# Performance work log

Measured on AMD Instinct MI355X. Metric: run time of the kernel, lower is better.

Reference implementation:

```python
import jax, jax.numpy as jnp
import numpy as np


def setup_inputs() -> dict:
    key = jax.random.key(0)
    k1, k2, k3, k4, k5 = jax.random.split(key, 5)
    M, K, N, E = 16384, 2048, 5632, 8  # total_tokens, d_model, expert ffn dim, num_experts
    a = jax.random.normal(k1, (M, K), jnp.float32) * 0.1          # fp8-valued activations (simulated in f32)
    b = jax.random.normal(k2, (E, N, K), jnp.float32) * 0.05      # column-major expert weights [E, N, K]
    scale_a = jax.random.uniform(k3, (M, 1), jnp.float32, 0.5, 1.5)   # per-token dequant scale
    scale_b = jax.random.uniform(k4, (E, 1), jnp.float32, 0.5, 1.5)   # per-expert dequant scale
    cuts = jnp.sort(jax.random.randint(k5, (E - 1,), 0, M)).astype(jnp.int32)
    seg_indptr = jnp.concatenate([jnp.zeros(1, jnp.int32), cuts, jnp.full((1,), M, jnp.int32)])
    return {"a": a, "b": b, "scale_a": scale_a, "scale_b": scale_b,
            "seg_indptr": seg_indptr, "batch_size": E}


def reference(a, b, scale_a, scale_b, seg_indptr, batch_size):
    # Grouped GEMM: for expert e, rows seg_indptr[e]:seg_indptr[e+1] of `a` are
    # multiplied by b[e]^T (b is column-major [E, N, K]).
    M = a.shape[0]
    E = b.shape[0]
    group_sizes = jnp.diff(seg_indptr).astype(jnp.int32)           # [E]
    out = jax.lax.ragged_dot(a, jnp.swapaxes(b, 1, 2), group_sizes)  # [M, N]
    # fp8 w8a8 dequant: per-token scale_a, per-expert scale_b gathered per token
    eid = jnp.clip(jnp.searchsorted(seg_indptr, jnp.arange(M), side='right') - 1, 0, E - 1)
    return out * scale_a * scale_b[eid]
```

## Files before the change

### kernel.cpp

```cpp
#include <hip/hip_runtime.h>


#define KSLICE 32
#define NSLICE 64
#define BM 256
#define BN 256

typedef __attribute__((ext_vector_type(4))) float f32x4;
typedef __attribute__((ext_vector_type(4))) unsigned int u32x4;
using frag_ab = __attribute__((ext_vector_type(8))) short;
using frag_cd = __attribute__((ext_vector_type(4))) float;

__device__ __forceinline__ unsigned int pack_bf2(float x, float y) {
  unsigned int ux = __float_as_uint(x);
  unsigned int uy = __float_as_uint(y);
  ux += 0x7fffu + ((ux >> 16) & 1u);
  uy += 0x7fffu + ((uy >> 16) & 1u);
  return (ux >> 16) | (uy & 0xffff0000u);
}

__device__ __forceinline__ void gload_lds16(const void* g, void* lds) {
  __builtin_amdgcn_global_load_lds(
      (const __attribute__((address_space(1))) unsigned int*)g,
      (__attribute__((address_space(3))) unsigned int*)lds, 16, 0, 0);
}

__global__ __launch_bounds__(256)
void convert_kernel(const float* __restrict__ A, const float* __restrict__ B,
                    unsigned short* __restrict__ wa, unsigned short* __restrict__ wb) {
  constexpr long long NA = 16384LL * 2048;
  constexpr long long NB = 8LL * 5632 * 2048;
  constexpr long long NA8 = NA / 8;
  constexpr long long NTOT = (NA + NB) / 8;
  for (long long c = (long long)blockIdx.x * 256 + threadIdx.x; c < NTOT;
       c += (long long)gridDim.x * 256) {
    const float* src;
    unsigned short* dst;
    long long off;
    if (c < NA8) { src = A; dst = wa; off = c * 8; }
    else         { src = B; dst = wb; off = (c - NA8) * 8; }
    f32x4 v0 = *(const f32x4*)(src + off);
    f32x4 v1 = *(const f32x4*)(src + off + 4);
    u32x4 o;
    o[0] = pack_bf2(v0[0], v0[1]);
    o[1] = pack_bf2(v0[2], v0[3]);
    o[2] = pack_bf2(v1[0], v1[1]);
    o[3] = pack_bf2(v1[2], v1[3]);
    *(u32x4*)(dst + off) = o;
  }
}

__global__ __launch_bounds__(512, 2)
void ggemm8(const unsigned short* __restrict__ A,
            const unsigned short* __restrict__ B,
            const float* __restrict__ sa,
            const float* __restrict__ sb,
            const int* __restrict__ seg,
            float* __restrict__ C) {
  constexpr int M = 16384, K = 2048, N = 5632, E = 8;
  constexpr int NT = N / BN;
  const int nwg = (M / BM) * NT;

  int bid = blockIdx.x;
  int sid = (bid & 7) * (nwg >> 3) + (bid >> 3);
  int mt = sid / NT, nt = sid % NT;
  int m0 = mt * BM, n0 = nt * BN;

  int tid = threadIdx.x;
  int lane = tid & 63;
  int w = tid >> 6;
  int wrow = (w >> 2) * 128;
  int wcol = (w & 3) * 64;
  int l16 = lane & 15, lhi = lane >> 4;

  __shared__ unsigned short Alds[4 * 8192];
  __shared__ unsigned short Blds[4 * 8192];

  int rpl = lane >> 3;
  int slog = (lane & 7) ^ rpl;
  int srow = rpl * 2 + (slog >> 2);
  int sk0 = (slog & 3) * 8;
  const unsigned short* gA0 = A + (size_t)(m0 + w * 32 + srow) * K + sk0;
  const unsigned short* gA1 = gA0 + (size_t)16 * K;
  unsigned short* ldsA0 = &Alds[(w * 2 + 0) * 512];
  unsigned short* ldsA1 = &Alds[(w * 2 + 1) * 512];
  unsigned short* ldsB0 = &Blds[(w * 2 + 0) * 512];
  unsigned short* ldsB1 = &Blds[(w * 2 + 1) * 512];

  int offA[8], offB[4];
#pragma unroll
  for (int i = 0; i < 8; ++i) {
    int r = wrow + i * 16 + l16;
    int rp = r >> 1;
    int sl = ((r & 1) << 2) | lhi;
    offA[i] = rp * 64 + ((sl ^ (rp & 7)) << 3);
  }
#pragma unroll
  for (int j = 0; j < 4; ++j) {
    int r = wcol + j * 16 + l16;
    int rp = r >> 1;
    int sl = ((r & 1) << 2) | lhi;
    offB[j] = rp * 64 + ((sl ^ (rp & 7)) << 3);
  }

  for (int e = 0; e < E; ++e) {
    int rlo = max(m0, seg[e]);
    int rhi = min(m0 + BM, seg[e + 1]);
    if (rlo >= rhi) continue;

    const unsigned short* gB0 =
        B + (size_t)e * N * K + (size_t)(n0 + w * 32 + srow) * K + sk0;
    const unsigned short* gB1 = gB0 + (size_t)16 * K;

    frag_cd acc[8][4];
#pragma unroll
    for (int i = 0; i < 8; ++i)
#pragma unroll
      for (int j = 0; j < 4; ++j) acc[i][j] = (frag_cd){0.f, 0.f, 0.f, 0.f};

    auto stage = [&](int s) {
      int slot = (s & 3) * 8192;
      int g = s * KSLICE;
      gload_lds16(gA0 + g, ldsA0 + slot);
      gload_lds16(gA1 + g, ldsA1 + slot);
      gload_lds16(gB0 + g, ldsB0 + slot);
      gload_lds16(gB1 + g, ldsB1 + slot);
    };

    auto phase = [&](int s, auto vmwait) {
      int slot = (s & 3) * 8192;
      frag_ab af[8], bf[4];
#pragma unroll
      for (int i = 0; i < 8; ++i)
        af[i] = *(const frag_ab*)(&Alds[slot + offA[i]]);
#pragma unroll
      for (int j = 0; j < 4; ++j)
        bf[j] = *(const frag_ab*)(&Blds[slot + offB[j]]);
      if (s + 3 < NSLICE) stage(s + 3);
      vmwait();
      __builtin_amdgcn_s_barrier();
      asm volatile("s_waitcnt lgkmcnt(0)" ::: "memory");
      __builtin_amdgcn_s_setprio(1);
#pragma unroll
      for (int i = 0; i < 8; ++i)
#pragma unroll
        for (int j = 0; j < 4; ++j)
          acc[i][j] = __builtin_amdgcn_mfma_f32_16x16x32_bf16(
              af[i], bf[j], acc[i][j], 0, 0, 0);
      __builtin_amdgcn_s_setprio(0);
      __builtin_amdgcn_s_barrier();
    };

    auto W8 = [] { asm volatile("s_waitcnt vmcnt(8)" ::: "memory"); };
    auto W4 = [] { asm volatile("s_waitcnt vmcnt(4)" ::: "memory"); };
    auto W0 = [] { asm volatile("s_waitcnt vmcnt(0)" ::: "memory"); };

    stage(0); stage(1); stage(2);
    asm volatile("s_waitcnt vmcnt(8)" ::: "memory");
    __builtin_amdgcn_s_barrier();

#pragma unroll 4
    for (int s = 0; s < NSLICE - 4; ++s) phase(s, W8);
    phase(NSLICE - 4, W8);
    phase(NSLICE - 3, W4);
    phase(NSLICE - 2, W0);
    phase(NSLICE - 1, W0);

    float sbe = sb[e];
#pragma unroll
    for (int i = 0; i < 8; ++i) {
#pragma unroll
      for (int r = 0; r < 4; ++r) {
        int grow = m0 + wrow + i * 16 + lhi * 4 + r;
        if (grow >= rlo && grow < rhi) {
          float s = sa[grow] * sbe;
          float* Crow = C + (size_t)grow * N + n0 + wcol;
#pragma unroll
          for (int j = 0; j < 4; ++j)
            Crow[j * 16 + l16] = acc[i][j][r] * s;
        }
      }
    }
  }
}

extern "C" void kernel_launch(void* const* d_in, const int* in_sizes, int n_in,
                              void* d_out, int out_size, void* d_ws, size_t ws_size,
                              hipStream_t stream) {
  const float* a = (const float*)d_in[0];
  const float* b = (const float*)d_in[1];
  const float* sa = (const float*)d_in[2];
  const float* sb = (const float*)d_in[3];
  const int* seg = (const int*)d_in[4];
  float* out = (float*)d_out;

  constexpr size_t NA = 16384ULL * 2048;
  constexpr size_t NB = 8ULL * 5632 * 2048;
  unsigned short* wa = (unsigned short*)d_ws;
  unsigned short* wb = wa + NA;

  hipLaunchKernelGGL(convert_kernel, dim3(2048), dim3(256), 0, stream, a, b, wa, wb);
  hipLaunchKernelGGL(ggemm8, dim3((16384 / BM) * (5632 / BN)), dim3(512), 0, stream,
                     wa, wb, sa, sb, seg, out);
}
```

Baseline: 790.2 us.

## Replace 256x256 deep-pipelined GEMM with simpler 128x128 double-buffered kernel

Swaps the 512-thread 256x256 tile kernel, which used a 4-slot LDS ring, hand-placed vmcnt waits and setprio, for a 256-thread 128x128 tile kernel. The new kernel uses 2-slot double buffering with __syncthreads and targets 3 blocks per CU. Smaller tiles give more workgroups and less wasted work on expert-boundary tiles. The cost is more global traffic per FLOP and a pipeline that hides less memory latency.

```diff
diff --git a/kernel.cpp b/kernel.cpp
--- a/kernel.cpp
+++ b/kernel.cpp
@@ -1,10 +1,9 @@
 #include <hip/hip_runtime.h>
 
 
-#define KSLICE 32
-#define NSLICE 64
-#define BM 256
-#define BN 256
+#define BK 32
+#define NKSTEP 64
+#define KDIM 2048
 
 typedef __attribute__((ext_vector_type(4))) float f32x4;
 typedef __attribute__((ext_vector_type(4))) unsigned int u32x4;
@@ -50,131 +49,94 @@
   }
 }
 
-__global__ __launch_bounds__(512, 2)
-void ggemm8(const unsigned short* __restrict__ A,
-            const unsigned short* __restrict__ B,
-            const float* __restrict__ sa,
-            const float* __restrict__ sb,
-            const int* __restrict__ seg,
-            float* __restrict__ C) {
-  constexpr int M = 16384, K = 2048, N = 5632, E = 8;
-  constexpr int NT = N / BN;
-  const int nwg = (M / BM) * NT;
+__global__ __launch_bounds__(256, 3)
+void ggemm_o(const unsigned short* __restrict__ A,
+             const unsigned short* __restrict__ B,
+             const float* __restrict__ sa,
+             const float* __restrict__ sb,
+             const int* __restrict__ seg,
+             float* __restrict__ C) {
+  constexpr int M = 16384, N = 5632, E = 8;
+  constexpr int NTC = N / 128;
+  const int nwg = (M / 128) * NTC;
 
   int bid = blockIdx.x;
   int sid = (bid & 7) * (nwg >> 3) + (bid >> 3);
-  int mt = sid / NT, nt = sid % NT;
-  int m0 = mt * BM, n0 = nt * BN;
+  int mt = sid / NTC, nt = sid % NTC;
+  int m0 = mt * 128, n0 = nt * 128;
 
-  int tid = threadIdx.x;
-  int lane = tid & 63;
-  int w = tid >> 6;
-  int wrow = (w >> 2) * 128;
-  int wcol = (w & 3) * 64;
+  int tid = threadIdx.x, lane = tid & 63, w = tid >> 6;
+  int wr = (w >> 1) * 64, wc = (w & 1) * 64;
   int l16 = lane & 15, lhi = lane >> 4;
 
-  __shared__ unsigned short Alds[4 * 8192];
-  __shared__ unsigned short Blds[4 * 8192];
+  __shared__ unsigned short Asm[2][128 * 32];
+  __shared__ unsigned short Bsm[2][128 * 32];
 
-  int rpl = lane >> 3;
-  int slog = (lane & 7) ^ rpl;
-  int srow = rpl * 2 + (slog >> 2);
-  int sk0 = (slog & 3) * 8;
-  const unsigned short* gA0 = A + (size_t)(m0 + w * 32 + srow) * K + sk0;
-  const unsigned short* gA1 = gA0 + (size_t)16 * K;
-  unsigned short* ldsA0 = &Alds[(w * 2 + 0) * 512];
-  unsigned short* ldsA1 = &Alds[(w * 2 + 1) * 512];
-  unsigned short* ldsB0 = &Blds[(w * 2 + 0) * 512];
-  unsigned short* ldsB1 = &Blds[(w * 2 + 1) * 512];
+  int sr = lane >> 2;
+  int scol = (((lane & 3) ^ (sr & 3)) * 8);
+  const unsigned short* gA = A + (size_t)(m0 + w * 32 + sr) * KDIM + scol;
 
-  int offA[8], offB[4];
+  int xA[4], xB[4];
 #pragma unroll
-  for (int i = 0; i < 8; ++i) {
-    int r = wrow + i * 16 + l16;
-    int rp = r >> 1;
-    int sl = ((r & 1) << 2) | lhi;
-    offA[i] = rp * 64 + ((sl ^ (rp & 7)) << 3);
-  }
+  for (int i = 0; i < 4; ++i)
+    xA[i] = (wr + i * 16 + l16) * 32 + ((lhi ^ (l16 & 3)) * 8);
 #pragma unroll
-  for (int j = 0; j < 4; ++j) {
-    int r = wcol + j * 16 + l16;
-    int rp = r >> 1;
-    int sl = ((r & 1) << 2) | lhi;
-    offB[j] = rp * 64 + ((sl ^ (rp & 7)) << 3);
-  }
+  for (int j = 0; j < 4; ++j)
+    xB[j] = (wc + j * 16 + l16) * 32 + ((lhi ^ (l16 & 3)) * 8);
 
   for (int e = 0; e < E; ++e) {
     int rlo = max(m0, seg[e]);
-    int rhi = min(m0 + BM, seg[e + 1]);
+    int rhi = min(m0 + 128, seg[e + 1]);
     if (rlo >= rhi) continue;
+    const unsigned short* gB =
+        B + (size_t)e * N * KDIM + (size_t)(n0 + w * 32 + sr) * KDIM + scol;
 
-    const unsigned short* gB0 =
-        B + (size_t)e * N * K + (size_t)(n0 + w * 32 + srow) * K + sk0;
-    const unsigned short* gB1 = gB0 + (size_t)16 * K;
-
-    frag_cd acc[8][4];
+    frag_cd acc[4][4];
 #pragma unroll
-    for (int i = 0; i < 8; ++i)
+    for (int i = 0; i < 4; ++i)
 #pragma unroll
       for (int j = 0; j < 4; ++j) acc[i][j] = (frag_cd){0.f, 0.f, 0.f, 0.f};
 
-    auto stage = [&](int s) {
-      int slot = (s & 3) * 8192;
-      int g = s * KSLICE;
-      gload_lds16(gA0 + g, ldsA0 + slot);
-      gload_lds16(gA1 + g, ldsA1 + slot);
-      gload_lds16(gB0 + g, ldsB0 + slot);
-      gload_lds16(gB1 + g, ldsB1 + slot);
+    auto stage = [&](int b, int kt) {
+#pragma unroll
+      for (int i = 0; i < 2; ++i) {
+        gload_lds16(gA + (size_t)i * 16 * KDIM + kt * BK,
+                    &Asm[b][(w * 32 + i * 16) * 32]);
+        gload_lds16(gB + (size_t)i * 16 * KDIM + kt * BK,
+                    &Bsm[b][(w * 32 + i * 16) * 32]);
+      }
     };
-
-    auto phase = [&](int s, auto vmwait) {
-      int slot = (s & 3) * 8192;
-      frag_ab af[8], bf[4];
+    auto compute = [&](int b) {
+      frag_ab af[4], bf[4];
 #pragma unroll
-      for (int i = 0; i < 8; ++i)
-        af[i] = *(const frag_ab*)(&Alds[slot + offA[i]]);
+      for (int i = 0; i < 4; ++i) af[i] = *(const frag_ab*)(&Asm[b][xA[i]]);
 #pragma unroll
-      for (int j = 0; j < 4; ++j)
-        bf[j] = *(const frag_ab*)(&Blds[slot + offB[j]]);
-      if (s + 3 < NSLICE) stage(s + 3);
-      vmwait();
-      __builtin_amdgcn_s_barrier();
-      asm volatile("s_waitcnt lgkmcnt(0)" ::: "memory");
-      __builtin_amdgcn_s_setprio(1);
+      for (int j = 0; j < 4; ++j) bf[j] = *(const frag_ab*)(&Bsm[b][xB[j]]);
 #pragma unroll
-      for (int i = 0; i < 8; ++i)
+      for (int i = 0; i < 4; ++i)
 #pragma unroll
         for (int j = 0; j < 4; ++j)
           acc[i][j] = __builtin_amdgcn_mfma_f32_16x16x32_bf16(
               af[i], bf[j], acc[i][j], 0, 0, 0);
-      __builtin_amdgcn_s_setprio(0);
-      __builtin_amdgcn_s_barrier();
     };
 
-    auto W8 = [] { asm volatile("s_waitcnt vmcnt(8)" ::: "memory"); };
-    auto W4 = [] { asm volatile("s_waitcnt vmcnt(4)" ::: "memory"); };
-    auto W0 = [] { asm volatile("s_waitcnt vmcnt(0)" ::: "memory"); };
-
-    stage(0); stage(1); stage(2);
-    asm volatile("s_waitcnt vmcnt(8)" ::: "memory");
-    __builtin_amdgcn_s_barrier();
-
-#pragma unroll 4
-    for (int s = 0; s < NSLICE - 4; ++s) phase(s, W8);
-    phase(NSLICE - 4, W8);
-    phase(NSLICE - 3, W4);
-    phase(NSLICE - 2, W0);
-    phase(NSLICE - 1, W0);
+    stage(0, 0);
+    __syncthreads();
+    for (int kt = 0; kt < NKSTEP; ++kt) {
+      if (kt + 1 < NKSTEP) stage((kt + 1) & 1, kt + 1);
+      compute(kt & 1);
+      __syncthreads();
+    }
 
     float sbe = sb[e];
 #pragma unroll
-    for (int i = 0; i < 8; ++i) {
+    for (int i = 0; i < 4; ++i) {
 #pragma unroll
       for (int r = 0; r < 4; ++r) {
-        int grow = m0 + wrow + i * 16 + lhi * 4 + r;
+        int grow = m0 + wr + i * 16 + lhi * 4 + r;
         if (grow >= rlo && grow < rhi) {
           float s = sa[grow] * sbe;
-          float* Crow = C + (size_t)grow * N + n0 + wcol;
+          float* Crow = C + (size_t)grow * N + n0 + wc;
 #pragma unroll
           for (int j = 0; j < 4; ++j)
             Crow[j * 16 + l16] = acc[i][j][r] * s;
@@ -195,11 +157,10 @@
   float* out = (float*)d_out;
 
   constexpr size_t NA = 16384ULL * 2048;
-  constexpr size_t NB = 8ULL * 5632 * 2048;
   unsigned short* wa = (unsigned short*)d_ws;
   unsigned short* wb = wa + NA;
 
   hipLaunchKernelGGL(convert_kernel, dim3(2048), dim3(256), 0, stream, a, b, wa, wb);
-  hipLaunchKernelGGL(ggemm8, dim3((16384 / BM) * (5632 / BN)), dim3(512), 0, stream,
+  hipLaunchKernelGGL(ggemm_o, dim3(5632), dim3(256), 0, stream,
                      wa, wb, sa, sb, seg, out);
 }
```

Measured after the change: 774.0 us. -2.0%, faster.
